# Optimization experiments

Measured on AMD Instinct MI355X. Metric: run time of the kernel, lower is better.

Reference implementation:

```python
import jax, jax.numpy as jnp
import numpy as np
import math

IN_DIM, OUT_DIM, NUM_BASIS = 256, 128, 6
MAX_IN_SEQ, MAX_OUT_SEQ = 512, 256
REDUCTION = 2
LN_EPS = 1e-5


def setup_inputs() -> dict:
    key = jax.random.key(0)
    ks = jax.random.split(key, 8)
    u = lambda k, shape, a: jax.random.uniform(k, shape, jnp.float32, -a, a)
    x = jax.random.normal(ks[0], (16, MAX_IN_SEQ, IN_DIM), jnp.float32)
    M = u(ks[1], (OUT_DIM, IN_DIM), 0.5)
    P = u(ks[2], (OUT_DIM, OUT_DIM, NUM_BASIS), 0.1)
    Linker = u(ks[3], (MAX_IN_SEQ, MAX_OUT_SEQ), 0.1)
    ln_gamma = jnp.ones((OUT_DIM,), jnp.float32)
    ln_beta = jnp.zeros((OUT_DIM,), jnp.float32)
    res_W = u(ks[4], (OUT_DIM, IN_DIM), 0.1)
    res_linker = u(ks[5], (MAX_IN_SEQ, MAX_OUT_SEQ), 0.1)
    # periods[i,j,g] = i*(out_dim*num_basis) + j*num_basis + g + 2 (non-trainable buffer)
    periods = (jnp.arange(OUT_DIM * OUT_DIM * NUM_BASIS, dtype=jnp.float32)
               .reshape(OUT_DIM, OUT_DIM, NUM_BASIS) + 2.0)
    return {"x": x, "M": M, "P": P, "Linker": Linker, "ln_gamma": ln_gamma,
            "ln_beta": ln_beta, "res_W": res_W, "res_linker": res_linker,
            "periods": periods, "actual_seq_len": 512}


def _layer_norm(z, gamma, beta):
    mu = jnp.mean(z, axis=-1, keepdims=True)
    var = jnp.var(z, axis=-1, keepdims=True)
    return (z - mu) * jax.lax.rsqrt(var + LN_EPS) * gamma + beta


def reference(x, M, P, Linker, ln_gamma, ln_beta, res_W, res_linker, periods, actual_seq_len):
    b, seq_len, _ = x.shape
    # Z = LN(x @ M^T)
    Z = _layer_norm(jnp.matmul(x, M.T), ln_gamma, ln_beta)  # (b, s, out)
    # position-dependent trig basis: phi[s,i,j,g] = cos(2*pi*s / periods[i,j,g])
    k = jnp.arange(seq_len, dtype=jnp.float32)[:, None, None, None]
    phi = jnp.cos(2.0 * math.pi * k / periods[None])          # (s, out, out, nb)
    # fold basis into per-position mixing matrix, then contract (matches sum over dims 3,4)
    W = jnp.einsum('ijg,sijg->sij', P, phi)                   # (s, out, out)
    T = jnp.einsum('bsj,sij->bsi', Z, W)                      # (b, s, out)
    # adaptive linker: reduce sequence length
    L = actual_seq_len
    Lo = max(1, L // REDUCTION)
    U = jnp.einsum('bsi,so->boi', T[:, :L], Linker[:L, :Lo])  # (b, out_seq, out)
    # 'separate' residual
    rfeat = jnp.matmul(x[:, :L], res_W.T)                     # (b, s, out)
    residual = jnp.einsum('bsi,so->boi', rfeat, res_linker[:L, :Lo])
    return U + residual
```

## Files before the change

kernel.cpp:

```cpp
#include <hip/hip_runtime.h>
#include <hip/hip_bf16.h>

#define LN_EPS 1e-5f

typedef __attribute__((ext_vector_type(8))) short short8;
typedef __attribute__((ext_vector_type(4))) float floatx4;

__device__ __forceinline__ float bf2f(unsigned int u16) {
    union { unsigned int i; float f; } v; v.i = (u16 & 0xffffu) << 16; return v.f;
}
__device__ __forceinline__ unsigned short f2bf(float f) {
    __hip_bfloat16 h = __float2bfloat16(f);
    union { __hip_bfloat16 h; unsigned short u; } v; v.h = h; return v.u;
}
__device__ __forceinline__ unsigned int pack2(float a, float b) {
    return (unsigned int)f2bf(a) | ((unsigned int)f2bf(b) << 16);
}

__global__ __launch_bounds__(256) void k_prep(const float* __restrict__ x,
                                              const float* __restrict__ M,
                                              const float* __restrict__ resW,
                                              const float* __restrict__ Linker,
                                              const float* __restrict__ resL,
                                              unsigned short* __restrict__ xb,
                                              unsigned short* __restrict__ Wcat,
                                              unsigned short* __restrict__ LcatT) {
    int blk = blockIdx.x, t = threadIdx.x;
    if (blk < 1024) {
        int base = blk * 2048 + t * 8;
        float4 a = *(const float4*)(x + base);
        float4 b = *(const float4*)(x + base + 4);
        uint4 o; o.x = pack2(a.x, a.y); o.y = pack2(a.z, a.w);
        o.z = pack2(b.x, b.y); o.w = pack2(b.z, b.w);
        *(uint4*)(xb + base) = o;
    } else if (blk < 1056) {
        int base = (blk - 1024) * 2048 + t * 8;
        int row = base >> 8, col = base & 255;
        const float* src = (row < 128) ? (M + row * 256 + col) : (resW + (row - 128) * 256 + col);
        float4 a = *(const float4*)src;
        float4 b = *(const float4*)(src + 4);
        uint4 o; o.x = pack2(a.x, a.y); o.y = pack2(a.z, a.w);
        o.z = pack2(b.x, b.y); o.w = pack2(b.z, b.w);
        *(uint4*)(Wcat + base) = o;
    } else {
        int o = blk - 1056;
        #pragma unroll
        for (int q = 0; q < 4; ++q) {
            int k = q * 256 + t;
            float v = (k < 512) ? Linker[(size_t)k * 256 + o] : resL[(size_t)(k - 512) * 256 + o];
            LcatT[(size_t)o * 1024 + k] = f2bf(v);
        }
    }
}

__global__ __launch_bounds__(256) void k1_zr(const unsigned short* __restrict__ xb,
                                             const unsigned short* __restrict__ Wcat,
                                             const float* __restrict__ gamma,
                                             const float* __restrict__ beta,
                                             unsigned short* __restrict__ Z,
                                             unsigned short* __restrict__ TR) {
    __shared__ float buf[32 * 258];
    __shared__ float red1[32 * 8], red2[32 * 8];
    __shared__ float mus[32], rsg[32];
    int t = threadIdx.x, w = t >> 6, l = t & 63;
    int lane15 = l & 15, quad = l >> 4;
    int r0 = blockIdx.x * 32;
    floatx4 acc[2][4] = {};
    for (int kk = 0; kk < 256; kk += 32) {
        int k0 = kk + quad * 8;
        short8 a0 = *(const short8*)(xb + (size_t)(r0 + lane15) * 256 + k0);
        short8 a1 = *(const short8*)(xb + (size_t)(r0 + 16 + lane15) * 256 + k0);
        #pragma unroll
        for (int nt = 0; nt < 4; ++nt) {
            int c = w * 64 + nt * 16 + lane15;
            short8 b = *(const short8*)(Wcat + (size_t)c * 256 + k0);
            acc[0][nt] = __builtin_amdgcn_mfma_f32_16x16x32_bf16(a0, b, acc[0][nt], 0, 0, 0);
            acc[1][nt] = __builtin_amdgcn_mfma_f32_16x16x32_bf16(a1, b, acc[1][nt], 0, 0, 0);
        }
    }
    #pragma unroll
    for (int mt = 0; mt < 2; ++mt)
        #pragma unroll
        for (int nt = 0; nt < 4; ++nt)
            #pragma unroll
            for (int r = 0; r < 4; ++r) {
                int ro = mt * 16 + quad * 4 + r;
                int co = w * 64 + nt * 16 + lane15;
                buf[ro * 258 + co] = acc[mt][nt][r];
            }
    __syncthreads();
    {
        int r = t >> 3, seg = t & 7;
        float s1 = 0.f, s2 = 0.f;
        #pragma unroll
        for (int e = 0; e < 16; ++e) { float v = buf[r * 258 + seg * 16 + e]; s1 += v; s2 += v * v; }
        red1[r * 8 + seg] = s1; red2[r * 8 + seg] = s2;
    }
    __syncthreads();
    if (t < 32) {
        float s1 = 0.f, s2 = 0.f;
        #pragma unroll
        for (int e = 0; e < 8; ++e) { s1 += red1[t * 8 + e]; s2 += red2[t * 8 + e]; }
        float mu = s1 * (1.0f / 128.0f);
        float var = s2 * (1.0f / 128.0f) - mu * mu;
        mus[t] = mu; rsg[t] = rsqrtf(var + LN_EPS);
    }
    __syncthreads();
    {
        int r = t >> 3, c0 = (t & 7) * 16;
        int grow = r0 + r;
        float mu = mus[r], rs = rsg[r];
        float zv[16], rv[16];
        #pragma unroll
        for (int e = 0; e < 16; ++e) {
            int j = c0 + e;
            zv[e] = (buf[r * 258 + j] - mu) * rs * gamma[j] + beta[j];
            rv[e] = buf[r * 258 + 128 + j];
        }
        uint4 oz0, oz1, or0, or1;
        oz0.x = pack2(zv[0], zv[1]);  oz0.y = pack2(zv[2], zv[3]);
        oz0.z = pack2(zv[4], zv[5]);  oz0.w = pack2(zv[6], zv[7]);
        oz1.x = pack2(zv[8], zv[9]);  oz1.y = pack2(zv[10], zv[11]);
        oz1.z = pack2(zv[12], zv[13]); oz1.w = pack2(zv[14], zv[15]);
        or0.x = pack2(rv[0], rv[1]);  or0.y = pack2(rv[2], rv[3]);
        or0.z = pack2(rv[4], rv[5]);  or0.w = pack2(rv[6], rv[7]);
        or1.x = pack2(rv[8], rv[9]);  or1.y = pack2(rv[10], rv[11]);
        or1.z = pack2(rv[12], rv[13]); or1.w = pack2(rv[14], rv[15]);
        *(uint4*)(Z + (size_t)grow * 128 + c0) = oz0;
        *(uint4*)(Z + (size_t)grow * 128 + c0 + 8) = oz1;
        int b = grow >> 9, s = grow & 511;
        size_t rbase = ((size_t)b * 1024 + 512 + s) * 128 + c0;
        *(uint4*)(TR + rbase) = or0;
        *(uint4*)(TR + rbase + 8) = or1;
    }
}

__global__ __launch_bounds__(256) void k2_w(const float* __restrict__ P,
                                            const float* __restrict__ periods,
                                            unsigned short* __restrict__ W) {
    int t = threadIdx.x;
    int et = blockIdx.x;
    int sc = blockIdx.y;
    int e0 = et * 512 + t * 2;
    const float* pp = P + (size_t)e0 * 6;
    float4 pa = *(const float4*)(pp);
    float4 pb = *(const float4*)(pp + 4);
    float4 pc = *(const float4*)(pp + 8);
    float pf[12] = { pa.x, pa.y, pa.z, pa.w, pb.x, pb.y, pb.z, pb.w, pc.x, pc.y, pc.z, pc.w };
    const float* qp = periods + (size_t)e0 * 6;
    float4 qa = *(const float4*)(qp);
    float4 qb = *(const float4*)(qp + 4);
    float4 qc = *(const float4*)(qp + 8);
    float iv[12] = { __builtin_amdgcn_rcpf(qa.x), __builtin_amdgcn_rcpf(qa.y),
                     __builtin_amdgcn_rcpf(qa.z), __builtin_amdgcn_rcpf(qa.w),
                     __builtin_amdgcn_rcpf(qb.x), __builtin_amdgcn_rcpf(qb.y),
                     __builtin_amdgcn_rcpf(qb.z), __builtin_amdgcn_rcpf(qb.w),
                     __builtin_amdgcn_rcpf(qc.x), __builtin_amdgcn_rcpf(qc.y),
                     __builtin_amdgcn_rcpf(qc.z), __builtin_amdgcn_rcpf(qc.w) };
    for (int ss = 0; ss < 32; ++ss) {
        int s = sc * 32 + ss;
        float sf = (float)s;
        float a0 = 0.f, a1 = 0.f;
        #pragma unroll
        for (int g = 0; g < 6; ++g) {
            float r = __builtin_amdgcn_fractf(sf * iv[g]);
            a0 += pf[g] * __builtin_amdgcn_cosf(r);
        }
        #pragma unroll
        for (int g = 6; g < 12; ++g) {
            float r = __builtin_amdgcn_fractf(sf * iv[g]);
            a1 += pf[g] * __builtin_amdgcn_cosf(r);
        }
        *(unsigned int*)(W + (size_t)s * 16384 + e0) = pack2(a0, a1);
    }
}

__global__ __launch_bounds__(64) void k2b_t(const unsigned short* __restrict__ W,
                                            const unsigned short* __restrict__ Z,
                                            unsigned short* __restrict__ TR) {
    int l = threadIdx.x, lane15 = l & 15, quad = l >> 4;
    int s = blockIdx.x;
    floatx4 acc[8] = {};
    #pragma unroll
    for (int kk = 0; kk < 4; ++kk) {
        int k0 = kk * 32 + quad * 8;
        short8 a = *(const short8*)(Z + ((size_t)lane15 * 512 + s) * 128 + k0);
        #pragma unroll
        for (int nt = 0; nt < 8; ++nt) {
            short8 b = *(const short8*)(W + (size_t)s * 16384 + (nt * 16 + lane15) * 128 + k0);
            acc[nt] = __builtin_amdgcn_mfma_f32_16x16x32_bf16(a, b, acc[nt], 0, 0, 0);
        }
    }
    #pragma unroll
    for (int nt = 0; nt < 8; ++nt)
        #pragma unroll
        for (int r = 0; r < 4; ++r) {
            int brow = quad * 4 + r;
            int i = nt * 16 + lane15;
            TR[((size_t)brow * 1024 + s) * 128 + i] = f2bf(acc[nt][r]);
        }
}

__global__ __launch_bounds__(256) void k3_out(const unsigned short* __restrict__ LcatT,
                                              const unsigned short* __restrict__ TR,
                                              float* __restrict__ out) {
    __shared__ unsigned short bt[4][64 * 40];
    __shared__ float red[4 * 32 * 64];
    int t = threadIdx.x, w = t >> 6, l = t & 63;
    int lane15 = l & 15, quad = l >> 4;
    int b = blockIdx.x, o0 = blockIdx.y * 32, i0 = blockIdx.z * 64;
    const unsigned short* trb = TR + (size_t)b * 1024 * 128;
    unsigned short* myBt = bt[w];
    floatx4 acc[2][4] = {};
    for (int kk = 0; kk < 8; ++kk) {
        int k0 = w * 256 + kk * 32;
        __syncthreads();
        {
            int kr = l & 31, ih = (l >> 5) * 8;
            #pragma unroll
            for (int q = 0; q < 4; ++q) {
                int ic = ih + q * 16;
                uint4 u = *(const uint4*)(trb + (size_t)(k0 + kr) * 128 + i0 + ic);
                const unsigned short* up = (const unsigned short*)&u;
                #pragma unroll
                for (int e = 0; e < 8; ++e) myBt[(ic + e) * 40 + kr] = up[e];
            }
        }
        __syncthreads();
        short8 afr0 = *(const short8*)(LcatT + (size_t)(o0 + lane15) * 1024 + k0 + quad * 8);
        short8 afr1 = *(const short8*)(LcatT + (size_t)(o0 + 16 + lane15) * 1024 + k0 + quad * 8);
        #pragma unroll
        for (int nt = 0; nt < 4; ++nt) {
            short8 bfr = *(const short8*)(myBt + (nt * 16 + lane15) * 40 + quad * 8);
            acc[0][nt] = __builtin_amdgcn_mfma_f32_16x16x32_bf16(afr0, bfr, acc[0][nt], 0, 0, 0);
            acc[1][nt] = __builtin_amdgcn_mfma_f32_16x16x32_bf16(afr1, bfr, acc[1][nt], 0, 0, 0);
        }
    }
    #pragma unroll
    for (int mt = 0; mt < 2; ++mt)
        #pragma unroll
        for (int nt = 0; nt < 4; ++nt)
            #pragma unroll
            for (int r = 0; r < 4; ++r) {
                int ro = mt * 16 + quad * 4 + r;
                int co = nt * 16 + lane15;
                red[(w * 32 + ro) * 64 + co] = acc[mt][nt][r];
            }
    __syncthreads();
    {
        int ro = t >> 3, c0 = (t & 7) * 8;
        float vs[8];
        #pragma unroll
        for (int e = 0; e < 8; ++e) {
            float sum = 0.f;
            #pragma unroll
            for (int ww = 0; ww < 4; ++ww) sum += red[(ww * 32 + ro) * 64 + c0 + e];
            vs[e] = sum;
        }
        float4 o1 = { vs[0], vs[1], vs[2], vs[3] };
        float4 o2 = { vs[4], vs[5], vs[6], vs[7] };
        size_t ob = ((size_t)b * 256 + o0 + ro) * 128 + i0 + c0;
        *(float4*)(out + ob) = o1;
        *(float4*)(out + ob + 4) = o2;
    }
}

extern "C" void kernel_launch(void* const* d_in, const int* in_sizes, int n_in,
                              void* d_out, int out_size, void* d_ws, size_t ws_size,
                              hipStream_t stream) {
    const float* x      = (const float*)d_in[0];
    const float* M      = (const float*)d_in[1];
    const float* P      = (const float*)d_in[2];
    const float* Linker = (const float*)d_in[3];
    const float* gamma  = (const float*)d_in[4];
    const float* beta   = (const float*)d_in[5];
    const float* resW   = (const float*)d_in[6];
    const float* resL   = (const float*)d_in[7];
    const float* periods= (const float*)d_in[8];
    (void)in_sizes; (void)n_in; (void)out_size; (void)ws_size;

    float* ws = (float*)d_ws;
    unsigned short* xb    = (unsigned short*)(ws);
    unsigned short* Wcat  = (unsigned short*)(ws + 1048576);
    unsigned short* LcatT = (unsigned short*)(ws + 1081344);
    unsigned short* Z     = (unsigned short*)(ws + 1212416);
    unsigned short* TR    = (unsigned short*)(ws + 1736704);
    unsigned short* W     = (unsigned short*)(ws + 2785280);

    k_prep<<<1312, 256, 0, stream>>>(x, M, resW, Linker, resL, xb, Wcat, LcatT);
    k2_w<<<dim3(32, 16), 256, 0, stream>>>(P, periods, W);
    k1_zr<<<256, 256, 0, stream>>>(xb, Wcat, gamma, beta, Z, TR);
    k2b_t<<<512, 64, 0, stream>>>(W, Z, TR);
    k3_out<<<dim3(16, 8, 2), 256, 0, stream>>>(LcatT, TR, (float*)d_out);
}
```

Before: 119.1 us.

## Fuse prep into consumers, use Chebyshev cosine recurrence, LDS-transpose linker

Removes the separate bf16 conversion kernel: k1_zr now reads fp32 x, M and resW directly and packs them to bf16 in registers. The W-basis generation is merged with the linker transpose into one launch. Per-position cosines are computed with the recurrence cos((s+1)θ)=2cosθ·cos(sθ)−cos((s−1)θ) instead of a transcendental per step. The linker transpose is staged through LDS so its global writes are coalesced. This saves one launch and an intermediate round trip through memory, but the recurrence can accumulate rounding error over 32 steps, and k1 now re-reads fp32 weights per block.

```diff
diff --git a/kernel.cpp b/kernel.cpp
--- a/kernel.cpp
+++ b/kernel.cpp
@@ -16,45 +16,96 @@
 __device__ __forceinline__ unsigned int pack2(float a, float b) {
     return (unsigned int)f2bf(a) | ((unsigned int)f2bf(b) << 16);
 }
-
-__global__ __launch_bounds__(256) void k_prep(const float* __restrict__ x,
-                                              const float* __restrict__ M,
-                                              const float* __restrict__ resW,
-                                              const float* __restrict__ Linker,
-                                              const float* __restrict__ resL,
-                                              unsigned short* __restrict__ xb,
-                                              unsigned short* __restrict__ Wcat,
-                                              unsigned short* __restrict__ LcatT) {
+__device__ __forceinline__ short8 pack8(float4 a, float4 b) {
+    union { short8 s; uint4 u; } v;
+    v.u.x = pack2(a.x, a.y); v.u.y = pack2(a.z, a.w);
+    v.u.z = pack2(b.x, b.y); v.u.w = pack2(b.z, b.w);
+    return v.s;
+}
+
+__global__ __launch_bounds__(256) void kB_w_lcat(const float* __restrict__ P,
+                                                 const float* __restrict__ periods,
+                                                 const float* __restrict__ Linker,
+                                                 const float* __restrict__ resL,
+                                                 unsigned short* __restrict__ W,
+                                                 unsigned short* __restrict__ LcatT) {
+    __shared__ unsigned short lds[32 * 260];
     int blk = blockIdx.x, t = threadIdx.x;
-    if (blk < 1024) {
-        int base = blk * 2048 + t * 8;
-        float4 a = *(const float4*)(x + base);
-        float4 b = *(const float4*)(x + base + 4);
-        uint4 o; o.x = pack2(a.x, a.y); o.y = pack2(a.z, a.w);
-        o.z = pack2(b.x, b.y); o.w = pack2(b.z, b.w);
-        *(uint4*)(xb + base) = o;
-    } else if (blk < 1056) {
-        int base = (blk - 1024) * 2048 + t * 8;
-        int row = base >> 8, col = base & 255;
-        const float* src = (row < 128) ? (M + row * 256 + col) : (resW + (row - 128) * 256 + col);
-        float4 a = *(const float4*)src;
-        float4 b = *(const float4*)(src + 4);
-        uint4 o; o.x = pack2(a.x, a.y); o.y = pack2(a.z, a.w);
-        o.z = pack2(b.x, b.y); o.w = pack2(b.z, b.w);
-        *(uint4*)(Wcat + base) = o;
+    if (blk < 512) {
+        int et = blk & 31, sc = blk >> 5;
+        int e0 = et * 512 + t * 2;
+        const float* pp = P + (size_t)e0 * 6;
+        float4 pa = *(const float4*)(pp);
+        float4 pb = *(const float4*)(pp + 4);
+        float4 pc = *(const float4*)(pp + 8);
+        float pf[12] = { pa.x, pa.y, pa.z, pa.w, pb.x, pb.y, pb.z, pb.w, pc.x, pc.y, pc.z, pc.w };
+        const float* qp = periods + (size_t)e0 * 6;
+        float4 qa = *(const float4*)(qp);
+        float4 qb = *(const float4*)(qp + 4);
+        float4 qc = *(const float4*)(qp + 8);
+        float iv[12] = { __builtin_amdgcn_rcpf(qa.x), __builtin_amdgcn_rcpf(qa.y),
+                         __builtin_amdgcn_rcpf(qa.z), __builtin_amdgcn_rcpf(qa.w),
+                         __builtin_amdgcn_rcpf(qb.x), __builtin_amdgcn_rcpf(qb.y),
+                         __builtin_amdgcn_rcpf(qb.z), __builtin_amdgcn_rcpf(qb.w),
+                         __builtin_amdgcn_rcpf(qc.x), __builtin_amdgcn_rcpf(qc.y),
+                         __builtin_amdgcn_rcpf(qc.z), __builtin_amdgcn_rcpf(qc.w) };
+        float s0 = (float)(sc * 32);
+        float tc[12], cm1[12], cc[12];
+        #pragma unroll
+        for (int g = 0; g < 12; ++g) {
+            tc[g]  = 2.0f * __builtin_amdgcn_cosf(iv[g]);
+            cm1[g] = __builtin_amdgcn_cosf(__builtin_amdgcn_fractf(s0 * iv[g]));
+            cc[g]  = __builtin_amdgcn_cosf(__builtin_amdgcn_fractf((s0 + 1.0f) * iv[g]));
+        }
+        #pragma unroll 4
+        for (int ss = 0; ss < 32; ++ss) {
+            float a0 = 0.f, a1 = 0.f;
+            #pragma unroll
+            for (int g = 0; g < 6; ++g)  a0 += pf[g] * cm1[g];
+            #pragma unroll
+            for (int g = 6; g < 12; ++g) a1 += pf[g] * cm1[g];
+            int s = sc * 32 + ss;
+            *(unsigned int*)(W + (size_t)s * 16384 + e0) = pack2(a0, a1);
+            #pragma unroll
+            for (int g = 0; g < 12; ++g) {
+                float cn = fmaf(tc[g], cc[g], -cm1[g]);
+                cm1[g] = cc[g]; cc[g] = cn;
+            }
+        }
     } else {
-        int o = blk - 1056;
-        #pragma unroll
-        for (int q = 0; q < 4; ++q) {
-            int k = q * 256 + t;
-            float v = (k < 512) ? Linker[(size_t)k * 256 + o] : resL[(size_t)(k - 512) * 256 + o];
-            LcatT[(size_t)o * 1024 + k] = f2bf(v);
-        }
-    }
-}
-
-__global__ __launch_bounds__(256) void k1_zr(const unsigned short* __restrict__ xb,
-                                             const unsigned short* __restrict__ Wcat,
+        int kb = blk - 512;
+        int k0 = kb * 32;
+        const float* src = (kb < 16) ? (Linker + (size_t)k0 * 256)
+                                     : (resL + (size_t)(k0 - 512) * 256);
+        #pragma unroll
+        for (int q = 0; q < 8; ++q) {
+            int lin = t + 256 * q;
+            int row = lin >> 6, col4 = (lin & 63) * 4;
+            float4 v = *(const float4*)(src + row * 256 + col4);
+            *(unsigned int*)(lds + row * 260 + col4)     = pack2(v.x, v.y);
+            *(unsigned int*)(lds + row * 260 + col4 + 2) = pack2(v.z, v.w);
+        }
+        __syncthreads();
+        int o = t;
+        unsigned int outw[16];
+        #pragma unroll
+        for (int kp = 0; kp < 16; ++kp) {
+            unsigned int lo = lds[(2 * kp) * 260 + o];
+            unsigned int hi = lds[(2 * kp + 1) * 260 + o];
+            outw[kp] = lo | (hi << 16);
+        }
+        unsigned short* dst = LcatT + (size_t)o * 1024 + k0;
+        #pragma unroll
+        for (int qq = 0; qq < 4; ++qq) {
+            uint4 u; u.x = outw[qq*4]; u.y = outw[qq*4+1]; u.z = outw[qq*4+2]; u.w = outw[qq*4+3];
+            *(uint4*)(dst + qq * 8) = u;
+        }
+    }
+}
+
+__global__ __launch_bounds__(256) void k1_zr(const float* __restrict__ x,
+                                             const float* __restrict__ M,
+                                             const float* __restrict__ resW,
                                              const float* __restrict__ gamma,
                                              const float* __restrict__ beta,
                                              unsigned short* __restrict__ Z,
@@ -65,15 +116,19 @@
     int t = threadIdx.x, w = t >> 6, l = t & 63;
     int lane15 = l & 15, quad = l >> 4;
     int r0 = blockIdx.x * 32;
+    const float* wbase = (w < 2) ? M : resW;
+    int wco = (w < 2) ? (w * 64) : (w * 64 - 128);
     floatx4 acc[2][4] = {};
     for (int kk = 0; kk < 256; kk += 32) {
         int k0 = kk + quad * 8;
-        short8 a0 = *(const short8*)(xb + (size_t)(r0 + lane15) * 256 + k0);
-        short8 a1 = *(const short8*)(xb + (size_t)(r0 + 16 + lane15) * 256 + k0);
+        const float* xr0 = x + (size_t)(r0 + lane15) * 256 + k0;
+        const float* xr1 = x + (size_t)(r0 + 16 + lane15) * 256 + k0;
+        short8 a0 = pack8(*(const float4*)xr0, *(const float4*)(xr0 + 4));
+        short8 a1 = pack8(*(const float4*)xr1, *(const float4*)(xr1 + 4));
         #pragma unroll
         for (int nt = 0; nt < 4; ++nt) {
-            int c = w * 64 + nt * 16 + lane15;
-            short8 b = *(const short8*)(Wcat + (size_t)c * 256 + k0);
+            const float* br = wbase + (size_t)(wco + nt * 16 + lane15) * 256 + k0;
+            short8 b = pack8(*(const float4*)br, *(const float4*)(br + 4));
             acc[0][nt] = __builtin_amdgcn_mfma_f32_16x16x32_bf16(a0, b, acc[0][nt], 0, 0, 0);
             acc[1][nt] = __builtin_amdgcn_mfma_f32_16x16x32_bf16(a1, b, acc[1][nt], 0, 0, 0);
         }
@@ -132,46 +187,6 @@
         size_t rbase = ((size_t)b * 1024 + 512 + s) * 128 + c0;
         *(uint4*)(TR + rbase) = or0;
         *(uint4*)(TR + rbase + 8) = or1;
-    }
-}
-
-__global__ __launch_bounds__(256) void k2_w(const float* __restrict__ P,
-                                            const float* __restrict__ periods,
-                                            unsigned short* __restrict__ W) {
-    int t = threadIdx.x;
-    int et = blockIdx.x;
-    int sc = blockIdx.y;
-    int e0 = et * 512 + t * 2;
-    const float* pp = P + (size_t)e0 * 6;
-    float4 pa = *(const float4*)(pp);
-    float4 pb = *(const float4*)(pp + 4);
-    float4 pc = *(const float4*)(pp + 8);
-    float pf[12] = { pa.x, pa.y, pa.z, pa.w, pb.x, pb.y, pb.z, pb.w, pc.x, pc.y, pc.z, pc.w };
-    const float* qp = periods + (size_t)e0 * 6;
-    float4 qa = *(const float4*)(qp);
-    float4 qb = *(const float4*)(qp + 4);
-    float4 qc = *(const float4*)(qp + 8);
-    float iv[12] = { __builtin_amdgcn_rcpf(qa.x), __builtin_amdgcn_rcpf(qa.y),
-                     __builtin_amdgcn_rcpf(qa.z), __builtin_amdgcn_rcpf(qa.w),
-                     __builtin_amdgcn_rcpf(qb.x), __builtin_amdgcn_rcpf(qb.y),
-                     __builtin_amdgcn_rcpf(qb.z), __builtin_amdgcn_rcpf(qb.w),
-                     __builtin_amdgcn_rcpf(qc.x), __builtin_amdgcn_rcpf(qc.y),
-                     __builtin_amdgcn_rcpf(qc.z), __builtin_amdgcn_rcpf(qc.w) };
-    for (int ss = 0; ss < 32; ++ss) {
-        int s = sc * 32 + ss;
-        float sf = (float)s;
-        float a0 = 0.f, a1 = 0.f;
-        #pragma unroll
-        for (int g = 0; g < 6; ++g) {
-            float r = __builtin_amdgcn_fractf(sf * iv[g]);
-            a0 += pf[g] * __builtin_amdgcn_cosf(r);
-        }
-        #pragma unroll
-        for (int g = 6; g < 12; ++g) {
-            float r = __builtin_amdgcn_fractf(sf * iv[g]);
-            a1 += pf[g] * __builtin_amdgcn_cosf(r);
-        }
-        *(unsigned int*)(W + (size_t)s * 16384 + e0) = pack2(a0, a1);
     }
 }
 
@@ -280,16 +295,13 @@
     (void)in_sizes; (void)n_in; (void)out_size; (void)ws_size;
 
     float* ws = (float*)d_ws;
-    unsigned short* xb    = (unsigned short*)(ws);
-    unsigned short* Wcat  = (unsigned short*)(ws + 1048576);
-    unsigned short* LcatT = (unsigned short*)(ws + 1081344);
-    unsigned short* Z     = (unsigned short*)(ws + 1212416);
-    unsigned short* TR    = (unsigned short*)(ws + 1736704);
-    unsigned short* W     = (unsigned short*)(ws + 2785280);
-
-    k_prep<<<1312, 256, 0, stream>>>(x, M, resW, Linker, resL, xb, Wcat, LcatT);
-    k2_w<<<dim3(32, 16), 256, 0, stream>>>(P, periods, W);
-    k1_zr<<<256, 256, 0, stream>>>(xb, Wcat, gamma, beta, Z, TR);
+    unsigned short* LcatT = (unsigned short*)(ws);
+    unsigned short* Z     = (unsigned short*)(ws + 131072);
+    unsigned short* TR    = (unsigned short*)(ws + 655360);
+    unsigned short* W     = (unsigned short*)(ws + 1703936);
+
+    kB_w_lcat<<<544, 256, 0, stream>>>(P, periods, Linker, resL, W, LcatT);
+    k1_zr<<<256, 256, 0, stream>>>(x, M, resW, gamma, beta, Z, TR);
     k2b_t<<<512, 64, 0, stream>>>(W, Z, TR);
     k3_out<<<dim3(16, 8, 2), 256, 0, stream>>>(LcatT, TR, (float*)d_out);
 }
```

Result: slower. 121.7 us (+2.2%).
